# Performance work log

Hardware: AMD Instinct MI355X
Metric: run time of the kernel (lower is better)

## Reference

```python
import jax, jax.numpy as jnp
import numpy as np

DISCOUNT_FACTOR = 0.99
AVERAGE_LAMBDA = 0.9
EPS = 1e-8
B, S = 8192, 2048


def setup_inputs() -> dict:
    key = jax.random.key(0)
    k1, k2, k3 = jax.random.split(key, 3)
    values = jax.random.normal(k1, (B, S + 1, 1), jnp.float32)
    rewards = jax.random.normal(k2, (B, S, 1), jnp.float32)
    # binary done flags stored as float, as in the torch module's math
    dones = (jax.random.uniform(k3, (B, S, 1)) < 0.02).astype(jnp.float32)
    # parameter init identical to GammaLambdaLearner.__init__ (atanh of targets)
    raw_gamma = jnp.arctanh(jnp.full((1,), DISCOUNT_FACTOR, jnp.float32))
    raw_lambd = jnp.arctanh(jnp.full((S,), AVERAGE_LAMBDA, jnp.float32))
    return {"values": values, "rewards": rewards, "dones": dones,
            "raw_gamma": raw_gamma, "raw_lambd": raw_lambd}


def reference(values, rewards, dones, raw_gamma, raw_lambd):
    # gamma / lambd properties: tanh then clamp_min(1e-8)
    gamma = jnp.maximum(jnp.tanh(raw_gamma), EPS)          # [1]
    lambd = jnp.maximum(jnp.tanh(raw_lambd), EPS)          # [S]

    # time-major views for the scan: [S, B, 1]
    r = jnp.swapaxes(rewards, 0, 1)
    d = jnp.swapaxes(dones, 0, 1)
    v_next = jnp.swapaxes(values[:, 1:], 0, 1)

    def step(carry, xs):
        # carry: lambda_return[t+1], shape [B, 1]
        r_t, d_t, vn_t, lam_t = xs
        ret = r_t + gamma * (1.0 - d_t) * ((1.0 - lam_t) * vn_t + lam_t * carry)
        return ret, ret

    # backward-in-time recurrence bootstrapped from the final value estimate
    _, outs = jax.lax.scan(step, values[:, -1], (r, d, v_next, lambd), reverse=True)
    return jnp.swapaxes(outs, 0, 1)  # [B, S, 1]
```

## Files before the change

kernel.cpp:

```cpp
#include <hip/hip_runtime.h>
#include <math.h>


#define EPSV 1e-8f

typedef float f32x4 __attribute__((ext_vector_type(4)));

__global__ void precompute_lambda_kernel(const float* __restrict__ raw_gamma,
                                         const float* __restrict__ raw_lambd,
                                         float* __restrict__ lam, int S) {
    int t = blockIdx.x * blockDim.x + threadIdx.x;
    if (t < S) lam[t] = fmaxf(tanhf(raw_lambd[t]), EPSV);
    if (t == S) lam[S] = fmaxf(tanhf(raw_gamma[0]), EPSV);
}

__device__ __forceinline__ void load_v4_nt(const float* __restrict__ vp,
                                           int s, int lane,
                                           const float* __restrict__ hi,
                                           float vv[4]) {
    const float* base = vp - s;
    f32x4 w = __builtin_nontemporal_load(reinterpret_cast<const f32x4*>(base));
    if (s == 0) { vv[0]=w[0]; vv[1]=w[1]; vv[2]=w[2]; vv[3]=w[3]; return; }
    float wn0 = __shfl_down(w[0], 1);
    float wn1 = __shfl_down(w[1], 1);
    float wn2 = __shfl_down(w[2], 1);
    if (lane == 63) {
        const float* p = base + 4;
        wn0 = (p + 0 < hi) ? p[0] : 0.0f;
        wn1 = (p + 1 < hi) ? p[1] : 0.0f;
        wn2 = (p + 2 < hi) ? p[2] : 0.0f;
    }
    if (s == 1)      { vv[0]=w[1]; vv[1]=w[2]; vv[2]=w[3]; vv[3]=wn0; }
    else if (s == 2) { vv[0]=w[2]; vv[1]=w[3]; vv[2]=wn0; vv[3]=wn1; }
    else             { vv[0]=w[3]; vv[1]=wn0; vv[2]=wn1; vv[3]=wn2; }
}

template <int NW>
__device__ __forceinline__ void block_suffix_scan(
    float A, float Bc, float* aggAs, float* aggBs, int lane, int wave,
    float& Af, float& Bf)
{
    float Ai = A, Bi = Bc;
    #pragma unroll
    for (int off = 1; off < 64; off <<= 1) {
        float Ao = __shfl_down(Ai, off);
        float Bo = __shfl_down(Bi, off);
        if (lane + off < 64) { Bi = fmaf(Ai, Bo, Bi); Ai = Ai * Ao; }
    }
    float Ae = __shfl_down(Ai, 1);
    float Be = __shfl_down(Bi, 1);
    if (lane == 63) { Ae = 1.0f; Be = 0.0f; }

    if (lane == 0) { aggAs[wave] = Ai; aggBs[wave] = Bi; }
    __syncthreads();
    float TA = 1.0f, TB = 0.0f;
    for (int w2 = wave + 1; w2 < NW; ++w2) {
        TB = fmaf(TA, aggBs[w2], TB);
        TA = TA * aggAs[w2];
    }
    Af = Ae * TA;
    Bf = fmaf(Ae, TB, Be);
}

__global__ __launch_bounds__(512) void lamret_kernel(
    const float* __restrict__ values,
    const float* __restrict__ rewards,
    const float* __restrict__ dones,
    const float* __restrict__ raw_gamma,
    const float* __restrict__ raw_lambd,
    const float* __restrict__ lam_pre,
    float* __restrict__ out,
    int S, long vtotal)
{
    __shared__ float aggA[8], aggB[8];

    const int row  = blockIdx.x;
    const int tid  = threadIdx.x;
    const int lane = tid & 63;
    const int wave = tid >> 6;

    const float* __restrict__ rrow = rewards + (size_t)row * S;
    const float* __restrict__ drow = dones   + (size_t)row * S;
    const float* __restrict__ vrow = values  + (size_t)row * (S + 1);
    float* __restrict__ orow = out + (size_t)row * S;

    float gamma;
    if (lam_pre) gamma = lam_pre[S];
    else         gamma = fmaxf(tanhf(raw_gamma[0]), EPSV);

    const float vlast = vrow[S];

    if (S == 2048) {
        constexpr int C = 4;
        const int t0 = tid * C;

        f32x4 r = __builtin_nontemporal_load(reinterpret_cast<const f32x4*>(rrow + t0));
        f32x4 d = __builtin_nontemporal_load(reinterpret_cast<const f32x4*>(drow + t0));

        const int s = (int)(((uintptr_t)(vrow + 1) >> 2) & 3);
        float vv[C];
        load_v4_nt(vrow + t0 + 1, s, lane, values + vtotal, vv);

        float lm[C];
        if (lam_pre) {
            f32x4 l = *reinterpret_cast<const f32x4*>(lam_pre + t0);
            #pragma unroll
            for (int i = 0; i < C; ++i) lm[i] = l[i];
        } else {
            #pragma unroll
            for (int i = 0; i < C; ++i) lm[i] = fmaxf(tanhf(raw_lambd[t0 + i]), EPSV);
        }

        float a[C], b[C];
        #pragma unroll
        for (int i = 0; i < C; ++i) {
            float g1d = gamma * (1.0f - d[i]);
            a[i] = g1d * lm[i];
            b[i] = fmaf(g1d * (1.0f - lm[i]), vv[i], r[i]);
        }

        float A = 1.0f, Bc = 0.0f;
        #pragma unroll
        for (int i = C - 1; i >= 0; --i) {
            Bc = fmaf(a[i], Bc, b[i]);
            A  = a[i] * A;
        }

        float Af, Bf;
        block_suffix_scan<8>(A, Bc, aggA, aggB, lane, wave, Af, Bf);
        float x = fmaf(Af, vlast, Bf);

        f32x4 o;
        #pragma unroll
        for (int i = C - 1; i >= 0; --i) {
            x = fmaf(a[i], x, b[i]);
            o[i] = x;
        }
        *reinterpret_cast<f32x4*>(orow + t0) = o;
    } else {
        constexpr int C = 8;
        const int t0 = tid * C;
        float a[C], b[C];
        #pragma unroll
        for (int i = 0; i < C; ++i) {
            int t = t0 + i;
            if (t < S) {
                float lmv = lam_pre ? lam_pre[t] : fmaxf(tanhf(raw_lambd[t]), EPSV);
                float g1d = gamma * (1.0f - drow[t]);
                a[i] = g1d * lmv;
                b[i] = fmaf(g1d * (1.0f - lmv), vrow[t + 1], rrow[t]);
            } else { a[i] = 1.0f; b[i] = 0.0f; }
        }
        float A = 1.0f, Bc = 0.0f;
        #pragma unroll
        for (int i = C - 1; i >= 0; --i) {
            Bc = fmaf(a[i], Bc, b[i]);
            A  = a[i] * A;
        }
        float Af, Bf;
        block_suffix_scan<8>(A, Bc, aggA, aggB, lane, wave, Af, Bf);
        float x = fmaf(Af, vlast, Bf);
        #pragma unroll
        for (int i = C - 1; i >= 0; --i) {
            x = fmaf(a[i], x, b[i]);
            if (t0 + i < S) orow[t0 + i] = x;
        }
    }
}

extern "C" void kernel_launch(void* const* d_in, const int* in_sizes, int n_in,
                              void* d_out, int out_size, void* d_ws, size_t ws_size,
                              hipStream_t stream) {
    const float* values    = (const float*)d_in[0];
    const float* rewards   = (const float*)d_in[1];
    const float* dones     = (const float*)d_in[2];
    const float* raw_gamma = (const float*)d_in[3];
    const float* raw_lambd = (const float*)d_in[4];
    float* out = (float*)d_out;

    const int S = in_sizes[4];
    const int B = in_sizes[1] / S;
    const long vtotal = in_sizes[0];

    float* lam_pre = nullptr;
    if (ws_size >= (size_t)(S + 1) * sizeof(float)) {
        lam_pre = (float*)d_ws;
        int nthr = 256;
        int nblk = (S + 1 + nthr - 1) / nthr;
        precompute_lambda_kernel<<<nblk, nthr, 0, stream>>>(raw_gamma, raw_lambd, lam_pre, S);
    }

    lamret_kernel<<<B, 512, 0, stream>>>(values, rewards, dones,
                                         raw_gamma, raw_lambd, lam_pre, out, S, vtotal);
}
```

Before: 210.1 us.

## Process four rows per block with software-pipelined prefetch of next row

Each block now handles four rows instead of one. It issues the loads for the next row before running the current row's block scan, and double-buffers the shared aggregates across iterations. The goal is to hide global load latency behind the scan's shuffles and barrier, and to reuse the lambda load across rows. In exchange the grid has four times fewer blocks, which lowers parallelism, and register use goes up from holding the prefetched loads.

```diff
diff --git a/kernel.cpp b/kernel.cpp
--- a/kernel.cpp
+++ b/kernel.cpp
@@ -14,18 +14,41 @@
     if (t == S) lam[S] = fmaxf(tanhf(raw_gamma[0]), EPSV);
 }
 
-__device__ __forceinline__ void load_v4_nt(const float* __restrict__ vp,
-                                           int s, int lane,
-                                           const float* __restrict__ hi,
-                                           float vv[4]) {
-    const float* base = vp - s;
-    f32x4 w = __builtin_nontemporal_load(reinterpret_cast<const f32x4*>(base));
+struct RowLoads {
+    f32x4 r, d, w;
+    float vlast;
+    const float* vbase;
+    int s;
+};
+
+__device__ __forceinline__ RowLoads issue_row(const float* __restrict__ values,
+                                              const float* __restrict__ rewards,
+                                              const float* __restrict__ dones,
+                                              int row, int S, int t0) {
+    RowLoads L;
+    const float* rrow = rewards + (size_t)row * S;
+    const float* drow = dones   + (size_t)row * S;
+    const float* vrow = values  + (size_t)row * (S + 1);
+    L.r = __builtin_nontemporal_load(reinterpret_cast<const f32x4*>(rrow + t0));
+    L.d = __builtin_nontemporal_load(reinterpret_cast<const f32x4*>(drow + t0));
+    L.s = (int)(((uintptr_t)(vrow + 1) >> 2) & 3);
+    L.vbase = vrow + t0 + 1 - L.s;
+    L.w = __builtin_nontemporal_load(reinterpret_cast<const f32x4*>(L.vbase));
+    L.vlast = vrow[S];
+    return L;
+}
+
+__device__ __forceinline__ void recombine_v(const RowLoads& L, int lane,
+                                            const float* __restrict__ hi,
+                                            float vv[4]) {
+    const f32x4 w = L.w;
+    const int s = L.s;
     if (s == 0) { vv[0]=w[0]; vv[1]=w[1]; vv[2]=w[2]; vv[3]=w[3]; return; }
     float wn0 = __shfl_down(w[0], 1);
     float wn1 = __shfl_down(w[1], 1);
     float wn2 = __shfl_down(w[2], 1);
     if (lane == 63) {
-        const float* p = base + 4;
+        const float* p = L.vbase + 4;
         wn0 = (p + 0 < hi) ? p[0] : 0.0f;
         wn1 = (p + 1 < hi) ? p[1] : 0.0f;
         wn2 = (p + 2 < hi) ? p[2] : 0.0f;
@@ -70,37 +93,25 @@
     const float* __restrict__ raw_lambd,
     const float* __restrict__ lam_pre,
     float* __restrict__ out,
-    int S, long vtotal)
+    int S, long vtotal, int B)
 {
-    __shared__ float aggA[8], aggB[8];
-
-    const int row  = blockIdx.x;
+    constexpr int ROWS = 4;
+    __shared__ float aggA[2][8], aggB[2][8];
+
     const int tid  = threadIdx.x;
     const int lane = tid & 63;
     const int wave = tid >> 6;
-
-    const float* __restrict__ rrow = rewards + (size_t)row * S;
-    const float* __restrict__ drow = dones   + (size_t)row * S;
-    const float* __restrict__ vrow = values  + (size_t)row * (S + 1);
-    float* __restrict__ orow = out + (size_t)row * S;
+    const int rbase = blockIdx.x * ROWS;
+    const float* const hi = values + vtotal;
 
     float gamma;
     if (lam_pre) gamma = lam_pre[S];
     else         gamma = fmaxf(tanhf(raw_gamma[0]), EPSV);
 
-    const float vlast = vrow[S];
-
     if (S == 2048) {
         constexpr int C = 4;
         const int t0 = tid * C;
 
-        f32x4 r = __builtin_nontemporal_load(reinterpret_cast<const f32x4*>(rrow + t0));
-        f32x4 d = __builtin_nontemporal_load(reinterpret_cast<const f32x4*>(drow + t0));
-
-        const int s = (int)(((uintptr_t)(vrow + 1) >> 2) & 3);
-        float vv[C];
-        load_v4_nt(vrow + t0 + 1, s, lane, values + vtotal, vv);
-
         float lm[C];
         if (lam_pre) {
             f32x4 l = *reinterpret_cast<const f32x4*>(lam_pre + t0);
@@ -111,59 +122,100 @@
             for (int i = 0; i < C; ++i) lm[i] = fmaxf(tanhf(raw_lambd[t0 + i]), EPSV);
         }
 
-        float a[C], b[C];
+        RowLoads cur;
+        if (rbase < B) cur = issue_row(values, rewards, dones, rbase, S, t0);
+
         #pragma unroll
-        for (int i = 0; i < C; ++i) {
-            float g1d = gamma * (1.0f - d[i]);
-            a[i] = g1d * lm[i];
-            b[i] = fmaf(g1d * (1.0f - lm[i]), vv[i], r[i]);
+        for (int k = 0; k < ROWS; ++k) {
+            const int row = rbase + k;
+            const bool valid = (row < B);
+
+            float a[C], b[C];
+            if (valid) {
+                float vv[C];
+                recombine_v(cur, lane, hi, vv);
+                #pragma unroll
+                for (int i = 0; i < C; ++i) {
+                    float g1d = gamma * (1.0f - cur.d[i]);
+                    a[i] = g1d * lm[i];
+                    b[i] = fmaf(g1d * (1.0f - lm[i]), vv[i], cur.r[i]);
+                }
+            } else {
+                #pragma unroll
+                for (int i = 0; i < C; ++i) { a[i] = 1.0f; b[i] = 0.0f; }
+            }
+            const float vlast = cur.vlast;
+
+            RowLoads nxt;
+            if (k + 1 < ROWS && row + 1 < B)
+                nxt = issue_row(values, rewards, dones, row + 1, S, t0);
+
+            float A = 1.0f, Bc = 0.0f;
+            #pragma unroll
+            for (int i = C - 1; i >= 0; --i) {
+                Bc = fmaf(a[i], Bc, b[i]);
+                A  = a[i] * A;
+            }
+
+            float Af, Bf;
+            block_suffix_scan<8>(A, Bc, aggA[k & 1], aggB[k & 1], lane, wave, Af, Bf);
+            float x = fmaf(Af, vlast, Bf);
+
+            if (valid) {
+                f32x4 o;
+                #pragma unroll
+                for (int i = C - 1; i >= 0; --i) {
+                    x = fmaf(a[i], x, b[i]);
+                    o[i] = x;
+                }
+                *reinterpret_cast<f32x4*>(out + (size_t)row * S + t0) = o;
+            }
+            cur = nxt;
         }
-
-        float A = 1.0f, Bc = 0.0f;
-        #pragma unroll
-        for (int i = C - 1; i >= 0; --i) {
-            Bc = fmaf(a[i], Bc, b[i]);
-            A  = a[i] * A;
-        }
-
-        float Af, Bf;
-        block_suffix_scan<8>(A, Bc, aggA, aggB, lane, wave, Af, Bf);
-        float x = fmaf(Af, vlast, Bf);
-
-        f32x4 o;
-        #pragma unroll
-        for (int i = C - 1; i >= 0; --i) {
-            x = fmaf(a[i], x, b[i]);
-            o[i] = x;
-        }
-        *reinterpret_cast<f32x4*>(orow + t0) = o;
     } else {
         constexpr int C = 8;
         const int t0 = tid * C;
-        float a[C], b[C];
-        #pragma unroll
-        for (int i = 0; i < C; ++i) {
-            int t = t0 + i;
-            if (t < S) {
-                float lmv = lam_pre ? lam_pre[t] : fmaxf(tanhf(raw_lambd[t]), EPSV);
-                float g1d = gamma * (1.0f - drow[t]);
-                a[i] = g1d * lmv;
-                b[i] = fmaf(g1d * (1.0f - lmv), vrow[t + 1], rrow[t]);
-            } else { a[i] = 1.0f; b[i] = 0.0f; }
-        }
-        float A = 1.0f, Bc = 0.0f;
-        #pragma unroll
-        for (int i = C - 1; i >= 0; --i) {
-            Bc = fmaf(a[i], Bc, b[i]);
-            A  = a[i] * A;
-        }
-        float Af, Bf;
-        block_suffix_scan<8>(A, Bc, aggA, aggB, lane, wave, Af, Bf);
-        float x = fmaf(Af, vlast, Bf);
-        #pragma unroll
-        for (int i = C - 1; i >= 0; --i) {
-            x = fmaf(a[i], x, b[i]);
-            if (t0 + i < S) orow[t0 + i] = x;
+        for (int k = 0; k < ROWS; ++k) {
+            const int row = rbase + k;
+            const bool valid = (row < B);
+            float a[C], b[C];
+            float vlast = 0.0f;
+            if (valid) {
+                const float* rrow = rewards + (size_t)row * S;
+                const float* drow = dones   + (size_t)row * S;
+                const float* vrow = values  + (size_t)row * (S + 1);
+                vlast = vrow[S];
+                #pragma unroll
+                for (int i = 0; i < C; ++i) {
+                    int t = t0 + i;
+                    if (t < S) {
+                        float lmv = lam_pre ? lam_pre[t] : fmaxf(tanhf(raw_lambd[t]), EPSV);
+                        float g1d = gamma * (1.0f - drow[t]);
+                        a[i] = g1d * lmv;
+                        b[i] = fmaf(g1d * (1.0f - lmv), vrow[t + 1], rrow[t]);
+                    } else { a[i] = 1.0f; b[i] = 0.0f; }
+                }
+            } else {
+                #pragma unroll
+                for (int i = 0; i < C; ++i) { a[i] = 1.0f; b[i] = 0.0f; }
+            }
+            float A = 1.0f, Bc = 0.0f;
+            #pragma unroll
+            for (int i = C - 1; i >= 0; --i) {
+                Bc = fmaf(a[i], Bc, b[i]);
+                A  = a[i] * A;
+            }
+            float Af, Bf;
+            block_suffix_scan<8>(A, Bc, aggA[k & 1], aggB[k & 1], lane, wave, Af, Bf);
+            float x = fmaf(Af, vlast, Bf);
+            if (valid) {
+                float* orow = out + (size_t)row * S;
+                #pragma unroll
+                for (int i = C - 1; i >= 0; --i) {
+                    x = fmaf(a[i], x, b[i]);
+                    if (t0 + i < S) orow[t0 + i] = x;
+                }
+            }
         }
     }
 }
@@ -190,6 +242,9 @@
         precompute_lambda_kernel<<<nblk, nthr, 0, stream>>>(raw_gamma, raw_lambd, lam_pre, S);
     }
 
-    lamret_kernel<<<B, 512, 0, stream>>>(values, rewards, dones,
-                                         raw_gamma, raw_lambd, lam_pre, out, S, vtotal);
-}
+    const int ROWS = 4;
+    int nblk = (B + ROWS - 1) / ROWS;
+    lamret_kernel<<<nblk, 512, 0, stream>>>(values, rewards, dones,
+                                            raw_gamma, raw_lambd, lam_pre, out,
+                                            S, vtotal, B);
+}
```

Result: no change. 209.2 us (-0.4%).
